# Kernel tuning notes

Measured on AMD Instinct MI355X. Metric: run time of the kernel, lower is better.

The kernel has to match this reference:

```python
import jax, jax.numpy as jnp
import numpy as np

NUM_HEADS = 16
HEAD_DIM = 64
LN_EPS = 1e-5


def setup_inputs() -> dict:
    key = jax.random.key(0)
    k1, k2, k3, k4 = jax.random.split(key, 4)
    B, N, D = 4, 2048, NUM_HEADS * HEAD_DIM
    q = jax.random.normal(k1, (B, N, D), dtype=jnp.float32)
    k = jax.random.normal(k2, (B, N, D), dtype=jnp.float32)
    v = jax.random.normal(k3, (B, N, D), dtype=jnp.float32)
    W_out = jax.random.normal(k4, (D, D), dtype=jnp.float32) * (1.0 / np.sqrt(D))
    g = jnp.ones((D,), dtype=jnp.float32)
    return {"q": q, "k": k, "v": v, "W_out": W_out, "g": g}


def _split_heads(x):
    b, n, _ = x.shape
    return x.reshape(b, n, NUM_HEADS, HEAD_DIM).transpose(0, 2, 1, 3)  # b h n d


def reference(q, k, v, W_out, g):
    scale = HEAD_DIM ** -0.5
    qh = _split_heads(q) * scale          # [b,h,n,d]
    kh = _split_heads(k)                  # [b,h,m,d]
    vh = _split_heads(v)                  # [b,h,m,d]
    sim = jnp.einsum('bhnd,bhmd->bhnm', qh, kh)
    attn = jax.nn.softmax(sim.astype(jnp.float32), axis=-1)
    out = jnp.einsum('bhnm,bhmd->bhnd', attn, vh)
    b, h, n, d = out.shape
    out = out.transpose(0, 2, 1, 3).reshape(b, n, h * d)  # b n (h d)
    out = out @ W_out.T                   # Linear, no bias
    # LayerNorm (bias=False), biased variance
    mean = jnp.mean(out, axis=-1, keepdims=True)
    var = jnp.var(out, axis=-1, keepdims=True)
    return (out - mean) * jax.lax.rsqrt(var + LN_EPS) * g
```

## Files before the change

kernel.cpp:

```cpp
#include <hip/hip_runtime.h>
#include <hip/hip_bf16.h>


#define Bv 4
#define Nv 2048
#define Hv 16
#define DHv 64
#define Dv 1024
#define NT (Nv / 64)

typedef __attribute__((ext_vector_type(8))) short short8;
typedef __attribute__((ext_vector_type(4))) float floatx4;

__device__ inline unsigned pack_bf2(float a, float b) {
    unsigned ua = __builtin_bit_cast(unsigned, a) + 0x8000u;
    unsigned ub = __builtin_bit_cast(unsigned, b) + 0x8000u;
    return __builtin_amdgcn_perm(ub, ua, 0x07060302u);
}

__global__ __launch_bounds__(256)
void attn_mfma(const float* __restrict__ q,
               const float* __restrict__ k,
               const float* __restrict__ v,
               __hip_bfloat16* __restrict__ out) {
    __shared__ __align__(16) short Kt[2][64 * 64];
    __shared__ __align__(16) short Vt[2][64 * 64];

    const int t = threadIdx.x;
    const int wave = t >> 6, lane = t & 63;
    const int quad = lane >> 4, lr = lane & 15;
    const int b = blockIdx.z, h = blockIdx.y;
    const int q0 = blockIdx.x * 128;
    const size_t bh = ((size_t)b * Nv) * Dv + h * DHv;

    float4 kpre[2][2], vpre[2][2];
    auto load_tile = [&](int k0) {
#pragma unroll
        for (int p = 0; p < 2; ++p) {
            int idx = p * 256 + t;
            int r = idx >> 3, cb = idx & 7;
            const float* kp = k + bh + (size_t)(k0 + r) * Dv + cb * 8;
            kpre[p][0] = *(const float4*)kp;
            kpre[p][1] = *(const float4*)(kp + 4);
            int dq = idx & 15, rr = idx >> 4;
            const float* vp = v + bh + (size_t)(k0 + 2 * rr) * Dv + dq * 4;
            vpre[p][0] = *(const float4*)vp;
            vpre[p][1] = *(const float4*)(vp + Dv);
        }
    };
    auto store_tile = [&](int buf) {
#pragma unroll
        for (int p = 0; p < 2; ++p) {
            int idx = p * 256 + t;
            int r = idx >> 3, cb = idx & 7;
            uint4 u;
            u.x = pack_bf2(kpre[p][0].x, kpre[p][0].y);
            u.y = pack_bf2(kpre[p][0].z, kpre[p][0].w);
            u.z = pack_bf2(kpre[p][1].x, kpre[p][1].y);
            u.w = pack_bf2(kpre[p][1].z, kpre[p][1].w);
            *(uint4*)&Kt[buf][r * 64 + ((cb ^ (r & 7)) << 3)] = u;
            int dq = idx & 15, rr = idx >> 4;
            float va[4] = {vpre[p][0].x, vpre[p][0].y, vpre[p][0].z, vpre[p][0].w};
            float vb[4] = {vpre[p][1].x, vpre[p][1].y, vpre[p][1].z, vpre[p][1].w};
#pragma unroll
            for (int i = 0; i < 4; ++i) {
                int d = dq * 4 + i;
                ((unsigned*)Vt[buf])[d * 32 + (((rr >> 2) ^ ((d >> 1) & 7)) << 2) + (rr & 3)] =
                    pack_bf2(va[i], vb[i]);
            }
        }
    };

    load_tile(0);

    short8 qfrag[2][2];
#pragma unroll
    for (int qs = 0; qs < 2; ++qs)
#pragma unroll
        for (int kh = 0; kh < 2; ++kh) {
            int row = q0 + wave * 32 + qs * 16 + lr;
            const float* qp = q + bh + (size_t)row * Dv + kh * 32 + quad * 8;
            float4 f0 = *(const float4*)qp;
            float4 f1 = *(const float4*)(qp + 4);
            int4 qi;
            qi.x = (int)pack_bf2(f0.x * 0.125f, f0.y * 0.125f);
            qi.y = (int)pack_bf2(f0.z * 0.125f, f0.w * 0.125f);
            qi.z = (int)pack_bf2(f1.x * 0.125f, f1.y * 0.125f);
            qi.w = (int)pack_bf2(f1.z * 0.125f, f1.w * 0.125f);
            qfrag[qs][kh] = __builtin_bit_cast(short8, qi);
        }

    store_tile(0);

    floatx4 o_acc[2][4] = {};
    float mrow[2] = {-INFINITY, -INFINITY};
    float lrow[2] = {0.f, 0.f};
    const int srcA = ((2 * (quad & 1)) << 4) | lr;
    const int srcB = srcA + 16;
    const bool hi = (quad >= 2);

    for (int it = 0; it < NT; ++it) {
        const int cur = it & 1;
        __syncthreads();
        if (it + 1 < NT) load_tile((it + 1) * 64);

        floatx4 s_acc[2][4] = {};
#pragma unroll
        for (int tt = 0; tt < 4; ++tt) {
            int row = tt * 16 + lr;
            short8 kf0 = *(const short8*)&Kt[cur][row * 64 + ((quad ^ (lr & 7)) << 3)];
            short8 kf1 = *(const short8*)&Kt[cur][row * 64 + (((4 + quad) ^ (lr & 7)) << 3)];
#pragma unroll
            for (int qs = 0; qs < 2; ++qs) {
                s_acc[qs][tt] = __builtin_amdgcn_mfma_f32_16x16x32_bf16(kf0, qfrag[qs][0], s_acc[qs][tt], 0, 0, 0);
                s_acc[qs][tt] = __builtin_amdgcn_mfma_f32_16x16x32_bf16(kf1, qfrag[qs][1], s_acc[qs][tt], 0, 0, 0);
            }
        }

        unsigned p2[2][8];
#pragma unroll
        for (int qs = 0; qs < 2; ++qs) {
            float tmax = -INFINITY;
#pragma unroll
            for (int tt = 0; tt < 4; ++tt)
#pragma unroll
                for (int r2 = 0; r2 < 4; ++r2) tmax = fmaxf(tmax, s_acc[qs][tt][r2]);
            tmax = fmaxf(tmax, __shfl_xor(tmax, 16));
            tmax = fmaxf(tmax, __shfl_xor(tmax, 32));
            float mnew = fmaxf(mrow[qs], tmax);
            float alpha = __expf(mrow[qs] - mnew);
            mrow[qs] = mnew;
            float psum = 0.f;
#pragma unroll
            for (int tt = 0; tt < 4; ++tt)
#pragma unroll
                for (int r2 = 0; r2 < 4; ++r2) {
                    float p = __expf(s_acc[qs][tt][r2] - mnew);
                    s_acc[qs][tt][r2] = p;
                    psum += p;
                }
            psum += __shfl_xor(psum, 16);
            psum += __shfl_xor(psum, 32);
            lrow[qs] = lrow[qs] * alpha + psum;
#pragma unroll
            for (int r2 = 0; r2 < 4; ++r2) {
                float ar = __shfl(alpha, quad * 4 + r2);
#pragma unroll
                for (int td = 0; td < 4; ++td) o_acc[qs][td][r2] *= ar;
            }
#pragma unroll
            for (int tt = 0; tt < 4; ++tt) {
                p2[qs][tt * 2 + 0] = pack_bf2(s_acc[qs][tt][0], s_acc[qs][tt][1]);
                p2[qs][tt * 2 + 1] = pack_bf2(s_acc[qs][tt][2], s_acc[qs][tt][3]);
            }
        }

#pragma unroll
        for (int kh = 0; kh < 2; ++kh) {
            short8 af[2];
#pragma unroll
            for (int qs = 0; qs < 2; ++qs) {
                int tlo = 4 * kh, thi = 4 * kh + 2;
                unsigned d0a = __shfl(p2[qs][tlo + 0], srcA), d0b = __shfl(p2[qs][thi + 0], srcA);
                unsigned d1a = __shfl(p2[qs][tlo + 1], srcA), d1b = __shfl(p2[qs][thi + 1], srcA);
                unsigned d2a = __shfl(p2[qs][tlo + 0], srcB), d2b = __shfl(p2[qs][thi + 0], srcB);
                unsigned d3a = __shfl(p2[qs][tlo + 1], srcB), d3b = __shfl(p2[qs][thi + 1], srcB);
                int4 afi;
                afi.x = (int)(hi ? d0b : d0a);
                afi.y = (int)(hi ? d1b : d1a);
                afi.z = (int)(hi ? d2b : d2a);
                afi.w = (int)(hi ? d3b : d3a);
                af[qs] = __builtin_bit_cast(short8, afi);
            }
#pragma unroll
            for (int td = 0; td < 4; ++td) {
                int d = td * 16 + lr;
                short8 vf = *(const short8*)&Vt[cur][d * 64 + (((kh * 4 + quad) ^ (lr >> 1)) << 3)];
                o_acc[0][td] = __builtin_amdgcn_mfma_f32_16x16x32_bf16(af[0], vf, o_acc[0][td], 0, 0, 0);
                o_acc[1][td] = __builtin_amdgcn_mfma_f32_16x16x32_bf16(af[1], vf, o_acc[1][td], 0, 0, 0);
            }
        }

        if (it + 1 < NT) store_tile(1 - cur);
    }

#pragma unroll
    for (int qs = 0; qs < 2; ++qs) {
        float linv = 1.f / lrow[qs];
#pragma unroll
        for (int r2 = 0; r2 < 4; ++r2) {
            float lv = __shfl(linv, quad * 4 + r2);
            int row = q0 + wave * 32 + qs * 16 + quad * 4 + r2;
            size_t base = ((size_t)(b * Nv + row)) * Dv + h * DHv;
#pragma unroll
            for (int td = 0; td < 4; ++td)
                out[base + td * 16 + lr] = __float2bfloat16(o_acc[qs][td][r2] * lv);
        }
    }
}

__global__ __launch_bounds__(256)
void wconv_kernel(const float* __restrict__ W, __hip_bfloat16* __restrict__ Wb) {
    int base = (blockIdx.x * 256 + threadIdx.x) * 8;
    float4 f0 = *(const float4*)(W + base);
    float4 f1 = *(const float4*)(W + base + 4);
    uint4 u;
    u.x = pack_bf2(f0.x, f0.y);
    u.y = pack_bf2(f0.z, f0.w);
    u.z = pack_bf2(f1.x, f1.y);
    u.w = pack_bf2(f1.z, f1.w);
    *(uint4*)(Wb + base) = u;
}

__global__ __launch_bounds__(256)
void proj_kernel(const __hip_bfloat16* __restrict__ A,
                 const __hip_bfloat16* __restrict__ Wb,
                 float* __restrict__ C) {
    __shared__ __align__(16) short As[2][128 * 64];
    __shared__ __align__(16) short Ws[2][128 * 64];

    const int t = threadIdx.x;
    const int wave = t >> 6, lane = t & 63;
    const int quad = lane >> 4, lr = lane & 15;
    const int wm = wave >> 1, wn = wave & 1;
    const int bm = blockIdx.y * 128;
    const int bn = blockIdx.x * 128;

    floatx4 acc[4][4] = {};

    auto stage = [&](int buf, int k0) {
#pragma unroll
        for (int c = 0; c < 4; ++c) {
            const int blk = c * 4 + wave;
            const int r = blk * 8 + (lane >> 3);
            const int g = (lane & 7) ^ (r & 7);
            const __hip_bfloat16* ga = A + (size_t)(bm + r) * Dv + k0 + g * 8;
            const __hip_bfloat16* gw = Wb + (size_t)(bn + r) * Dv + k0 + g * 8;
            __builtin_amdgcn_global_load_lds(
                (const __attribute__((address_space(1))) unsigned int*)(const void*)ga,
                (__attribute__((address_space(3))) unsigned int*)(void*)&As[buf][blk * 512],
                16, 0, 0);
            __builtin_amdgcn_global_load_lds(
                (const __attribute__((address_space(1))) unsigned int*)(const void*)gw,
                (__attribute__((address_space(3))) unsigned int*)(void*)&Ws[buf][blk * 512],
                16, 0, 0);
        }
    };

    stage(0, 0);

    for (int it = 0; it < Dv / 64; ++it) {
        const int cur = it & 1;
        __syncthreads();
        if (it + 1 < Dv / 64) stage(1 - cur, (it + 1) * 64);

#pragma unroll
        for (int ks = 0; ks < 2; ++ks) {
            short8 af[4];
#pragma unroll
            for (int mb = 0; mb < 4; ++mb) {
                int row = wm * 64 + mb * 16 + lr;
                af[mb] = *(const short8*)&As[cur][row * 64 + (((ks * 4 + quad) ^ (lr & 7)) << 3)];
            }
#pragma unroll
            for (int nb = 0; nb < 4; ++nb) {
                int row = wn * 64 + nb * 16 + lr;
                short8 bf = *(const short8*)&Ws[cur][row * 64 + (((ks * 4 + quad) ^ (lr & 7)) << 3)];
#pragma unroll
                for (int mb = 0; mb < 4; ++mb)
                    acc[mb][nb] = __builtin_amdgcn_mfma_f32_16x16x32_bf16(af[mb], bf, acc[mb][nb], 0, 0, 0);
            }
        }
    }

#pragma unroll
    for (int mb = 0; mb < 4; ++mb)
#pragma unroll
        for (int nb = 0; nb < 4; ++nb) {
            int row = bm + wm * 64 + mb * 16 + quad * 4;
            int col = bn + wn * 64 + nb * 16 + lr;
#pragma unroll
            for (int r = 0; r < 4; ++r)
                C[(size_t)(row + r) * Dv + col] = acc[mb][nb][r];
        }
}

__global__ __launch_bounds__(256)
void proj_kernel_f32w(const __hip_bfloat16* __restrict__ A,
                      const float* __restrict__ W,
                      float* __restrict__ C) {
    __shared__ __align__(16) short As[2][128 * 32];
    __shared__ __align__(16) short Ws[2][128 * 32];

    const int t = threadIdx.x;
    const int wave = t >> 6, lane = t & 63;
    const int quad = lane >> 4, lr = lane & 15;
    const int wm = wave >> 1, wn = wave & 1;
    const int bm = blockIdx.y * 128;
    const int bn = blockIdx.x * 128;

    floatx4 acc[4][4] = {};

    const int rA = t >> 2;
    const int cbA = t & 3;

    uint4 apre[2];
    float4 wpre[2][2];
    auto load_t = [&](int k0) {
#pragma unroll
        for (int p = 0; p < 2; ++p) {
            int r = rA + p * 64;
            apre[p] = *(const uint4*)(A + (size_t)(bm + r) * Dv + k0 + cbA * 8);
            const float* wp = W + (size_t)(bn + r) * Dv + k0 + cbA * 8;
            wpre[p][0] = *(const float4*)wp;
            wpre[p][1] = *(const float4*)(wp + 4);
        }
    };
    auto store_t = [&](int buf) {
#pragma unroll
        for (int p = 0; p < 2; ++p) {
            int r = rA + p * 64;
            *(uint4*)&As[buf][r * 32 + cbA * 8] = apre[p];
            uint4 u;
            u.x = pack_bf2(wpre[p][0].x, wpre[p][0].y);
            u.y = pack_bf2(wpre[p][0].z, wpre[p][0].w);
            u.z = pack_bf2(wpre[p][1].x, wpre[p][1].y);
            u.w = pack_bf2(wpre[p][1].z, wpre[p][1].w);
            *(uint4*)&Ws[buf][r * 32 + cbA * 8] = u;
        }
    };

    load_t(0);
    store_t(0);

    for (int it = 0; it < Dv / 32; ++it) {
        const int cur = it & 1;
        __syncthreads();
        if (it + 1 < Dv / 32) load_t((it + 1) * 32);

        short8 af[4];
#pragma unroll
        for (int mb = 0; mb < 4; ++mb)
            af[mb] = *(const short8*)&As[cur][(wm * 64 + mb * 16 + lr) * 32 + quad * 8];
#pragma unroll
        for (int nb = 0; nb < 4; ++nb) {
            short8 bf = *(const short8*)&Ws[cur][(wn * 64 + nb * 16 + lr) * 32 + quad * 8];
#pragma unroll
            for (int mb = 0; mb < 4; ++mb)
                acc[mb][nb] = __builtin_amdgcn_mfma_f32_16x16x32_bf16(af[mb], bf, acc[mb][nb], 0, 0, 0);
        }

        if (it + 1 < Dv / 32) store_t(1 - cur);
    }

#pragma unroll
    for (int mb = 0; mb < 4; ++mb)
#pragma unroll
        for (int nb = 0; nb < 4; ++nb) {
            int row = bm + wm * 64 + mb * 16 + quad * 4;
            int col = bn + wn * 64 + nb * 16 + lr;
#pragma unroll
            for (int r = 0; r < 4; ++r)
                C[(size_t)(row + r) * Dv + col] = acc[mb][nb][r];
        }
}

__global__ __launch_bounds__(256)
void ln_kernel(float* __restrict__ C,
               const float* __restrict__ g) {
    const int row = blockIdx.x;
    const int t = threadIdx.x;
    const int wave = t >> 6, lane = t & 63;

    float* rp = C + (size_t)row * Dv;
    float4 x = *(const float4*)(rp + t * 4);

    float s = x.x + x.y + x.z + x.w;
    float sq = x.x * x.x + x.y * x.y + x.z * x.z + x.w * x.w;
#pragma unroll
    for (int off = 32; off >= 1; off >>= 1) {
        s += __shfl_xor(s, off);
        sq += __shfl_xor(sq, off);
    }
    __shared__ float ss[4], ssq[4];
    if (lane == 0) { ss[wave] = s; ssq[wave] = sq; }
    __syncthreads();
    s = ss[0] + ss[1] + ss[2] + ss[3];
    sq = ssq[0] + ssq[1] + ssq[2] + ssq[3];

    const float rn = 1.f / (float)Dv;
    float mean = s * rn;
    float var = sq * rn - mean * mean;
    float inv = rsqrtf(var + 1e-5f);

    float4 gv = *(const float4*)(g + t * 4);

    float4 o;
    o.x = (x.x - mean) * inv * gv.x;
    o.y = (x.y - mean) * inv * gv.y;
    o.z = (x.z - mean) * inv * gv.z;
    o.w = (x.w - mean) * inv * gv.w;
    *(float4*)(rp + t * 4) = o;
}

extern "C" void kernel_launch(void* const* d_in, const int* in_sizes, int n_in,
                              void* d_out, int out_size, void* d_ws, size_t ws_size,
                              hipStream_t stream) {
    const float* q = (const float*)d_in[0];
    const float* k = (const float*)d_in[1];
    const float* v = (const float*)d_in[2];
    const float* W = (const float*)d_in[3];
    const float* g = (const float*)d_in[4];
    float* out = (float*)d_out;

    const size_t attnBytes = (size_t)Bv * Nv * Dv * 2;
    const size_t wbBytes = (size_t)Dv * Dv * 2;

    __hip_bfloat16* attn = (__hip_bfloat16*)d_ws;

    attn_mfma<<<dim3(Nv / 128, Hv, Bv), 256, 0, stream>>>(q, k, v, attn);

    if (ws_size >= attnBytes + wbBytes) {
        __hip_bfloat16* Wb = (__hip_bfloat16*)((char*)d_ws + attnBytes);
        wconv_kernel<<<512, 256, 0, stream>>>(W, Wb);
        proj_kernel<<<dim3(Dv / 128, (Bv * Nv) / 128), 256, 0, stream>>>(attn, Wb, out);
    } else {
        proj_kernel_f32w<<<dim3(Dv / 128, (Bv * Nv) / 128), 256, 0, stream>>>(attn, W, out);
    }

    ln_kernel<<<Bv * Nv, 256, 0, stream>>>(out, g);
}
```

Baseline: 318.8 us.

## Precompute bf16 K and transposed bf16 V, stream them into LDS directly

Adds a prep pass that converts K (and W) to bf16 and a kernel that transposes V per head into bf16, so the attention kernel can stage K and V tiles with direct global-to-LDS loads instead of re-reading and converting fp32 in every query block. The proj and attention kernels also remap block indices so neighbouring tiles land on the same XCD for L2 reuse. The cost is two extra passes over K and V plus more workspace, and the new path runs only when the workspace is large enough.

```diff
diff --git a/kernel.cpp b/kernel.cpp
--- a/kernel.cpp
+++ b/kernel.cpp
@@ -16,6 +16,234 @@
     unsigned ua = __builtin_bit_cast(unsigned, a) + 0x8000u;
     unsigned ub = __builtin_bit_cast(unsigned, b) + 0x8000u;
     return __builtin_amdgcn_perm(ub, ua, 0x07060302u);
+}
+
+#define KCONV_BLOCKS 4096
+#define WCONV_BLOCKS 512
+
+__global__ __launch_bounds__(256)
+void prep_conv(const float* __restrict__ K, __hip_bfloat16* __restrict__ Kb,
+               const float* __restrict__ W, __hip_bfloat16* __restrict__ Wb) {
+    const float* src;
+    __hip_bfloat16* dst;
+    int bid = blockIdx.x;
+    if (bid < KCONV_BLOCKS) { src = K; dst = Kb; }
+    else { src = W; dst = Wb; bid -= KCONV_BLOCKS; }
+    int base = (bid * 256 + threadIdx.x) * 8;
+    float4 f0 = *(const float4*)(src + base);
+    float4 f1 = *(const float4*)(src + base + 4);
+    uint4 u;
+    u.x = pack_bf2(f0.x, f0.y);
+    u.y = pack_bf2(f0.z, f0.w);
+    u.z = pack_bf2(f1.x, f1.y);
+    u.w = pack_bf2(f1.z, f1.w);
+    *(uint4*)(dst + base) = u;
+}
+
+__global__ __launch_bounds__(256)
+void wconv_kernel(const float* __restrict__ W, __hip_bfloat16* __restrict__ Wb) {
+    int base = (blockIdx.x * 256 + threadIdx.x) * 8;
+    float4 f0 = *(const float4*)(W + base);
+    float4 f1 = *(const float4*)(W + base + 4);
+    uint4 u;
+    u.x = pack_bf2(f0.x, f0.y);
+    u.y = pack_bf2(f0.z, f0.w);
+    u.z = pack_bf2(f1.x, f1.y);
+    u.w = pack_bf2(f1.z, f1.w);
+    *(uint4*)(Wb + base) = u;
+}
+
+__global__ __launch_bounds__(256)
+void vtrans_kernel(const float* __restrict__ v, __hip_bfloat16* __restrict__ vt) {
+    __shared__ short T[64][72];
+    const int b = blockIdx.z, h = blockIdx.y, n0 = blockIdx.x * 64;
+    const int t = threadIdx.x;
+    const int ir = t >> 4;
+    const int d4 = (t & 15) * 4;
+#pragma unroll
+    for (int pass = 0; pass < 4; ++pass) {
+        int n = pass * 16 + ir;
+        float4 f = *(const float4*)(v + ((size_t)b * Nv + n0 + n) * Dv + h * DHv + d4);
+        T[d4 + 0][n] = (short)(pack_bf2(f.x, f.x) & 0xffffu);
+        T[d4 + 1][n] = (short)(pack_bf2(f.y, f.y) & 0xffffu);
+        T[d4 + 2][n] = (short)(pack_bf2(f.z, f.z) & 0xffffu);
+        T[d4 + 3][n] = (short)(pack_bf2(f.w, f.w) & 0xffffu);
+    }
+    __syncthreads();
+    const int d = t >> 2, kg = (t & 3) * 16;
+    unsigned u[8];
+#pragma unroll
+    for (int i = 0; i < 8; ++i)
+        u[i] = (unsigned)(unsigned short)T[d][kg + 2 * i] |
+               ((unsigned)(unsigned short)T[d][kg + 2 * i + 1] << 16);
+    __hip_bfloat16* op = vt + ((size_t)(b * Hv + h) * DHv + d) * Nv + n0 + kg;
+    *(uint4*)op = *(uint4*)&u[0];
+    *(uint4*)(op + 8) = *(uint4*)&u[4];
+}
+
+__global__ __launch_bounds__(256)
+void attn_mfma_pre(const float* __restrict__ q,
+                   const __hip_bfloat16* __restrict__ Kb,
+                   const __hip_bfloat16* __restrict__ Vtb,
+                   __hip_bfloat16* __restrict__ out) {
+    __shared__ __align__(16) short Kt[2][64 * 64];
+    __shared__ __align__(16) short Vt[2][64 * 64];
+
+    const int t = threadIdx.x;
+    const int wave = t >> 6, lane = t & 63;
+    const int quad = lane >> 4, lr = lane & 15;
+    const int b = blockIdx.z;
+    const int lid2 = blockIdx.y * 16 + blockIdx.x;
+    const int xcd = lid2 & 7, jj = lid2 >> 3;
+    const int h = xcd * 2 + (jj >> 4);
+    const int q0 = (jj & 15) * 128;
+    const size_t qbh = ((size_t)b * Nv) * Dv + h * DHv;
+    const __hip_bfloat16* kb = Kb + (size_t)b * Nv * Dv + h * DHv;
+    const __hip_bfloat16* vtb = Vtb + (size_t)(b * Hv + h) * DHv * Nv;
+
+    const int srow = lane >> 3;
+    const int sg = lane & 7;
+    auto stage = [&](int buf, int k0) {
+#pragma unroll
+        for (int c = 0; c < 2; ++c) {
+            int blk = wave * 2 + c;
+            int r = blk * 8 + srow;
+            int g = sg ^ (r & 7);
+            __builtin_amdgcn_global_load_lds(
+                (const __attribute__((address_space(1))) unsigned*)(const void*)
+                    (kb + (size_t)(k0 + r) * Dv + g * 8),
+                (__attribute__((address_space(3))) unsigned*)(void*)&Kt[buf][blk * 512],
+                16, 0, 0);
+            __builtin_amdgcn_global_load_lds(
+                (const __attribute__((address_space(1))) unsigned*)(const void*)
+                    (vtb + (size_t)r * Nv + k0 + g * 8),
+                (__attribute__((address_space(3))) unsigned*)(void*)&Vt[buf][blk * 512],
+                16, 0, 0);
+        }
+    };
+
+    stage(0, 0);
+
+    short8 qfrag[2][2];
+#pragma unroll
+    for (int qs = 0; qs < 2; ++qs)
+#pragma unroll
+        for (int kh = 0; kh < 2; ++kh) {
+            int row = q0 + wave * 32 + qs * 16 + lr;
+            const float* qp = q + qbh + (size_t)row * Dv + kh * 32 + quad * 8;
+            float4 f0 = *(const float4*)qp;
+            float4 f1 = *(const float4*)(qp + 4);
+            int4 qi;
+            qi.x = (int)pack_bf2(f0.x * 0.125f, f0.y * 0.125f);
+            qi.y = (int)pack_bf2(f0.z * 0.125f, f0.w * 0.125f);
+            qi.z = (int)pack_bf2(f1.x * 0.125f, f1.y * 0.125f);
+            qi.w = (int)pack_bf2(f1.z * 0.125f, f1.w * 0.125f);
+            qfrag[qs][kh] = __builtin_bit_cast(short8, qi);
+        }
+
+    floatx4 o_acc[2][4] = {};
+    float mrow[2] = {-INFINITY, -INFINITY};
+    float lrow[2] = {0.f, 0.f};
+    const int srcA = ((2 * (quad & 1)) << 4) | lr;
+    const int srcB = srcA + 16;
+    const bool hi = (quad >= 2);
+
+    for (int it = 0; it < NT; ++it) {
+        const int cur = it & 1;
+        __syncthreads();
+        if (it + 1 < NT) stage(1 - cur, (it + 1) * 64);
+
+        floatx4 s_acc[2][4] = {};
+#pragma unroll
+        for (int tt = 0; tt < 4; ++tt) {
+            int row = tt * 16 + lr;
+            short8 kf0 = *(const short8*)&Kt[cur][row * 64 + ((quad ^ (lr & 7)) << 3)];
+            short8 kf1 = *(const short8*)&Kt[cur][row * 64 + (((4 + quad) ^ (lr & 7)) << 3)];
+#pragma unroll
+            for (int qs = 0; qs < 2; ++qs) {
+                s_acc[qs][tt] = __builtin_amdgcn_mfma_f32_16x16x32_bf16(kf0, qfrag[qs][0], s_acc[qs][tt], 0, 0, 0);
+                s_acc[qs][tt] = __builtin_amdgcn_mfma_f32_16x16x32_bf16(kf1, qfrag[qs][1], s_acc[qs][tt], 0, 0, 0);
+            }
+        }
+
+        unsigned p2[2][8];
+#pragma unroll
+        for (int qs = 0; qs < 2; ++qs) {
+            float tmax = -INFINITY;
+#pragma unroll
+            for (int tt = 0; tt < 4; ++tt)
+#pragma unroll
+                for (int r2 = 0; r2 < 4; ++r2) tmax = fmaxf(tmax, s_acc[qs][tt][r2]);
+            tmax = fmaxf(tmax, __shfl_xor(tmax, 16));
+            tmax = fmaxf(tmax, __shfl_xor(tmax, 32));
+            float mnew = fmaxf(mrow[qs], tmax);
+            float alpha = __expf(mrow[qs] - mnew);
+            mrow[qs] = mnew;
+            float psum = 0.f;
+#pragma unroll
+            for (int tt = 0; tt < 4; ++tt)
+#pragma unroll
+                for (int r2 = 0; r2 < 4; ++r2) {
+                    float p = __expf(s_acc[qs][tt][r2] - mnew);
+                    s_acc[qs][tt][r2] = p;
+                    psum += p;
+                }
+            psum += __shfl_xor(psum, 16);
+            psum += __shfl_xor(psum, 32);
+            lrow[qs] = lrow[qs] * alpha + psum;
+#pragma unroll
+            for (int r2 = 0; r2 < 4; ++r2) {
+                float ar = __shfl(alpha, quad * 4 + r2);
+#pragma unroll
+                for (int td = 0; td < 4; ++td) o_acc[qs][td][r2] *= ar;
+            }
+#pragma unroll
+            for (int tt = 0; tt < 4; ++tt) {
+                p2[qs][tt * 2 + 0] = pack_bf2(s_acc[qs][tt][0], s_acc[qs][tt][1]);
+                p2[qs][tt * 2 + 1] = pack_bf2(s_acc[qs][tt][2], s_acc[qs][tt][3]);
+            }
+        }
+
+#pragma unroll
+        for (int kh = 0; kh < 2; ++kh) {
+            short8 af[2];
+#pragma unroll
+            for (int qs = 0; qs < 2; ++qs) {
+                int tlo = 4 * kh, thi = 4 * kh + 2;
+                unsigned d0a = __shfl(p2[qs][tlo + 0], srcA), d0b = __shfl(p2[qs][thi + 0], srcA);
+                unsigned d1a = __shfl(p2[qs][tlo + 1], srcA), d1b = __shfl(p2[qs][thi + 1], srcA);
+                unsigned d2a = __shfl(p2[qs][tlo + 0], srcB), d2b = __shfl(p2[qs][thi + 0], srcB);
+                unsigned d3a = __shfl(p2[qs][tlo + 1], srcB), d3b = __shfl(p2[qs][thi + 1], srcB);
+                int4 afi;
+                afi.x = (int)(hi ? d0b : d0a);
+                afi.y = (int)(hi ? d1b : d1a);
+                afi.z = (int)(hi ? d2b : d2a);
+                afi.w = (int)(hi ? d3b : d3a);
+                af[qs] = __builtin_bit_cast(short8, afi);
+            }
+#pragma unroll
+            for (int td = 0; td < 4; ++td) {
+                int d = td * 16 + lr;
+                short8 vf = *(const short8*)&Vt[cur][d * 64 + (((kh * 4 + quad) ^ (lr & 7)) << 3)];
+                o_acc[0][td] = __builtin_amdgcn_mfma_f32_16x16x32_bf16(af[0], vf, o_acc[0][td], 0, 0, 0);
+                o_acc[1][td] = __builtin_amdgcn_mfma_f32_16x16x32_bf16(af[1], vf, o_acc[1][td], 0, 0, 0);
+            }
+        }
+    }
+
+#pragma unroll
+    for (int qs = 0; qs < 2; ++qs) {
+        float linv = 1.f / lrow[qs];
+#pragma unroll
+        for (int r2 = 0; r2 < 4; ++r2) {
+            float lv = __shfl(linv, quad * 4 + r2);
+            int row = q0 + wave * 32 + qs * 16 + quad * 4 + r2;
+            size_t base = ((size_t)(b * Nv + row)) * Dv + h * DHv;
+#pragma unroll
+            for (int td = 0; td < 4; ++td)
+                out[base + td * 16 + lr] = __float2bfloat16(o_acc[qs][td][r2] * lv);
+        }
+    }
 }
 
 __global__ __launch_bounds__(256)
@@ -200,19 +428,6 @@
 }
 
 __global__ __launch_bounds__(256)
-void wconv_kernel(const float* __restrict__ W, __hip_bfloat16* __restrict__ Wb) {
-    int base = (blockIdx.x * 256 + threadIdx.x) * 8;
-    float4 f0 = *(const float4*)(W + base);
-    float4 f1 = *(const float4*)(W + base + 4);
-    uint4 u;
-    u.x = pack_bf2(f0.x, f0.y);
-    u.y = pack_bf2(f0.z, f0.w);
-    u.z = pack_bf2(f1.x, f1.y);
-    u.w = pack_bf2(f1.z, f1.w);
-    *(uint4*)(Wb + base) = u;
-}
-
-__global__ __launch_bounds__(256)
 void proj_kernel(const __hip_bfloat16* __restrict__ A,
                  const __hip_bfloat16* __restrict__ Wb,
                  float* __restrict__ C) {
@@ -223,8 +438,10 @@
     const int wave = t >> 6, lane = t & 63;
     const int quad = lane >> 4, lr = lane & 15;
     const int wm = wave >> 1, wn = wave & 1;
-    const int bm = blockIdx.y * 128;
-    const int bn = blockIdx.x * 128;
+    const int lid = blockIdx.y * 8 + blockIdx.x;
+    const int xcd = lid & 7, j = lid >> 3;
+    const int bm = (xcd * 8 + (j >> 3)) * 128;
+    const int bn = (j & 7) * 128;
 
     floatx4 acc[4][4] = {};
 
@@ -413,18 +630,28 @@
     const float* g = (const float*)d_in[4];
     float* out = (float*)d_out;
 
-    const size_t attnBytes = (size_t)Bv * Nv * Dv * 2;
-    const size_t wbBytes = (size_t)Dv * Dv * 2;
+    const size_t attnB = (size_t)Bv * Nv * Dv * 2;
+    const size_t wbB = (size_t)Dv * Dv * 2;
+    const size_t kbB = (size_t)Bv * Nv * Dv * 2;
+    const size_t vtB = (size_t)Bv * Hv * DHv * Nv * 2;
 
     __hip_bfloat16* attn = (__hip_bfloat16*)d_ws;
 
-    attn_mfma<<<dim3(Nv / 128, Hv, Bv), 256, 0, stream>>>(q, k, v, attn);
-
-    if (ws_size >= attnBytes + wbBytes) {
-        __hip_bfloat16* Wb = (__hip_bfloat16*)((char*)d_ws + attnBytes);
-        wconv_kernel<<<512, 256, 0, stream>>>(W, Wb);
+    if (ws_size >= attnB + wbB + kbB + vtB) {
+        __hip_bfloat16* Wb = (__hip_bfloat16*)((char*)d_ws + attnB);
+        __hip_bfloat16* Kb = (__hip_bfloat16*)((char*)d_ws + attnB + wbB);
+        __hip_bfloat16* Vtb = (__hip_bfloat16*)((char*)d_ws + attnB + wbB + kbB);
+        prep_conv<<<KCONV_BLOCKS + WCONV_BLOCKS, 256, 0, stream>>>(k, Kb, W, Wb);
+        vtrans_kernel<<<dim3(Nv / 64, Hv, Bv), 256, 0, stream>>>(v, Vtb);
+        attn_mfma_pre<<<dim3(16, 16, Bv), 256, 0, stream>>>(q, Kb, Vtb, attn);
+        proj_kernel<<<dim3(Dv / 128, (Bv * Nv) / 128), 256, 0, stream>>>(attn, Wb, out);
+    } else if (ws_size >= attnB + wbB) {
+        __hip_bfloat16* Wb = (__hip_bfloat16*)((char*)d_ws + attnB);
+        wconv_kernel<<<WCONV_BLOCKS, 256, 0, stream>>>(W, Wb);
+        attn_mfma<<<dim3(Nv / 128, Hv, Bv), 256, 0, stream>>>(q, k, v, attn);
         proj_kernel<<<dim3(Dv / 128, (Bv * Nv) / 128), 256, 0, stream>>>(attn, Wb, out);
     } else {
+        attn_mfma<<<dim3(Nv / 128, Hv, Bv), 256, 0, stream>>>(q, k, v, attn);
         proj_kernel_f32w<<<dim3(Dv / 128, (Bv * Nv) / 128), 256, 0, stream>>>(attn, W, out);
     }
 
```

Result: slower. 341.0 us (+7.0%).
